# Performance work log

Measured on AMD Instinct MI355X. Metric: run time of the kernel, lower is better.

The kernel has to match this reference:

```python
import jax, jax.numpy as jnp
import numpy as np

N_NODES = 50000
N_EDGES = 400000
F_IN = 128
HID = 64
HEADS = 8
N_CLASSES = 16
NEG_SLOPE = 0.2  # PyG GATConv default negative_slope


def _glorot(key, shape):
    fan_in, fan_out = shape[0], shape[-1]
    lim = jnp.sqrt(6.0 / (fan_in + fan_out))
    return jax.random.uniform(key, shape, jnp.float32, -lim, lim)


def setup_inputs() -> dict:
    key = jax.random.key(0)
    ks = jax.random.split(key, 16)
    x = jax.random.normal(ks[0], (N_NODES, F_IN), jnp.float32)
    edge_index = jax.random.randint(ks[1], (2, N_EDGES), 0, N_NODES, jnp.int64)
    # layer 0: F_IN -> HEADS*HID (concat)
    W0 = _glorot(ks[2], (F_IN, HEADS * HID))
    a_s0 = _glorot(ks[3], (HEADS, HID))
    a_d0 = _glorot(ks[4], (HEADS, HID))
    b0 = jnp.zeros((HEADS * HID,), jnp.float32)
    # layer 1: HEADS*HID -> HEADS*HID (concat)
    W1 = _glorot(ks[5], (HEADS * HID, HEADS * HID))
    a_s1 = _glorot(ks[6], (HEADS, HID))
    a_d1 = _glorot(ks[7], (HEADS, HID))
    b1 = jnp.zeros((HEADS * HID,), jnp.float32)
    # final layer: HEADS*HID -> N_CLASSES, heads=1, concat=False (mean over heads)
    W2 = _glorot(ks[8], (HEADS * HID, 1 * N_CLASSES))
    a_s2 = _glorot(ks[9], (1, N_CLASSES))
    a_d2 = _glorot(ks[10], (1, N_CLASSES))
    b2 = jnp.zeros((N_CLASSES,), jnp.float32)
    return {"x": x, "edge_index": edge_index,
            "W0": W0, "a_s0": a_s0, "a_d0": a_d0, "b0": b0,
            "W1": W1, "a_s1": a_s1, "a_d1": a_d1, "b1": b1,
            "W2": W2, "a_s2": a_s2, "a_d2": a_d2, "b2": b2}


def gat_conv(x, src, dst, W, a_src, a_dst, b, num_nodes, concat):
    """One PyG-style GATConv (self-loops already in src/dst).
    x: [N, F_in]; W: [F_in, H*C]; a_src/a_dst: [H, C]; b: [H*C] or [C]."""
    H, C = a_src.shape
    h = (x @ W).reshape(num_nodes, H, C)                    # [N,H,C]
    al_s = jnp.einsum('nhc,hc->nh', h, a_src)               # [N,H]
    al_d = jnp.einsum('nhc,hc->nh', h, a_dst)               # [N,H]
    e = jax.nn.leaky_relu(al_s[src] + al_d[dst], NEG_SLOPE) # [E,H]
    # scatter-softmax over incoming edges of each destination node
    m = jax.ops.segment_max(e, dst, num_segments=num_nodes)  # [N,H]
    ex = jnp.exp(e - m[dst])
    denom = jax.ops.segment_sum(ex, dst, num_segments=num_nodes)
    alpha = ex / denom[dst]                                  # [E,H]
    out = jax.ops.segment_sum(alpha[:, :, None] * h[src], dst,
                              num_segments=num_nodes)        # [N,H,C]
    if concat:
        return out.reshape(num_nodes, H * C) + b
    return out.mean(axis=1) + b


def reference(x, edge_index, W0, a_s0, a_d0, b0, W1, a_s1, a_d1, b1,
              W2, a_s2, a_d2, b2):
    N = x.shape[0]
    # PyG GATConv adds self-loops by default
    loops = jnp.arange(N, dtype=edge_index.dtype)
    src = jnp.concatenate([edge_index[0], loops])
    dst = jnp.concatenate([edge_index[1], loops])
    h = gat_conv(x, src, dst, W0, a_s0, a_d0, b0, N, concat=True)
    h = jax.nn.elu(h)  # dropout is identity in eval mode
    h = gat_conv(h, src, dst, W1, a_s1, a_d1, b1, N, concat=True)
    h = jax.nn.elu(h)
    return gat_conv(h, src, dst, W2, a_s2, a_d2, b2, N, concat=False)
```

## Files before the change

### kernel.cpp

```cpp
#include <hip/hip_runtime.h>

#define N_NODES 50000
#define N_EDGES 400000
#define E_TOT   450000
#define NEG 0.2f
#define NB_SCAN ((N_NODES + 255) / 256)
#define MAXD 64

typedef unsigned short ushort_t;
typedef __attribute__((ext_vector_type(8))) _Float16 half8;
typedef __attribute__((ext_vector_type(4))) float  f32x4;
typedef __attribute__((ext_vector_type(8))) unsigned short ushort8;

__device__ __forceinline__ ushort_t f2h(float f){
    _Float16 h = (_Float16)f;
    union { _Float16 h; ushort_t u; } v; v.h = h; return v.u;
}
__device__ __forceinline__ float h_lo(unsigned u){
    union { unsigned u; _Float16 h[2]; } v; v.u = u; return (float)v.h[0];
}
__device__ __forceinline__ float h_hi(unsigned u){
    union { unsigned u; _Float16 h[2]; } v; v.u = u; return (float)v.h[1];
}
__device__ __forceinline__ void gload_lds16(const void* g, void* l){
    __builtin_amdgcn_global_load_lds((const __attribute__((address_space(1))) void*)g,
                                     (__attribute__((address_space(3))) void*)l, 16, 0, 0);
}
__device__ __forceinline__ int wave_incl_scan(int v, int lane){
    #pragma unroll
    for(int off = 1; off < 64; off <<= 1){
        int t = __shfl_up(v, off, 64);
        if(lane >= off) v += t;
    }
    return v;
}


__global__ void zero_ints(int* p, int n){
    int i = blockIdx.x*256 + threadIdx.x;
    if(i < n) p[i] = 0;
}

__global__ void count_deg(const int* __restrict__ ei, int* __restrict__ deg){
    int e = blockIdx.x*256 + threadIdx.x;
    if(e >= E_TOT) return;
    int dst = (e < N_EDGES) ? ei[N_EDGES + e] : (e - N_EDGES);
    atomicAdd(&deg[dst], 1);
}

__global__ void deg_block_sum(const int* __restrict__ deg, int* __restrict__ bsum){
    int i = blockIdx.x*256 + threadIdx.x;
    int lane = threadIdx.x & 63, wave = threadIdx.x >> 6;
    int v = (i < N_NODES) ? deg[i] : 0;
    #pragma unroll
    for(int off = 1; off < 64; off <<= 1) v += __shfl_xor(v, off, 64);
    __shared__ int sw[4];
    if(lane == 0) sw[wave] = v;
    __syncthreads();
    if(threadIdx.x == 0) bsum[blockIdx.x] = sw[0] + sw[1] + sw[2] + sw[3];
}

__global__ void scan_bsum(int* __restrict__ bsum, int* __restrict__ rowptr){
    int lane = threadIdx.x & 63, wave = threadIdx.x >> 6;
    int v = (threadIdx.x < NB_SCAN) ? bsum[threadIdx.x] : 0;
    int incl = wave_incl_scan(v, lane);
    __shared__ int sw[4];
    if(lane == 63) sw[wave] = incl;
    __syncthreads();
    int add = 0;
    for(int w = 0; w < wave; w++) add += sw[w];
    int excl = incl - v + add;
    if(threadIdx.x < NB_SCAN) bsum[threadIdx.x] = excl;
    if(threadIdx.x == 255) rowptr[N_NODES] = excl + v;
}

__global__ void scan_apply(const int* __restrict__ bsum,
                           int* __restrict__ dw, int* __restrict__ rowptr){
    int i = blockIdx.x*256 + threadIdx.x;
    int lane = threadIdx.x & 63, wave = threadIdx.x >> 6;
    int v = (i < N_NODES) ? dw[i] : 0;
    int incl = wave_incl_scan(v, lane);
    __shared__ int sw[4];
    if(lane == 63) sw[wave] = incl;
    __syncthreads();
    int add = bsum[blockIdx.x];
    for(int w = 0; w < wave; w++) add += sw[w];
    int excl = incl - v + add;
    if(i < N_NODES){ rowptr[i] = excl; dw[i] = excl; }
}

__global__ void scatter_edges(const int* __restrict__ ei, int* __restrict__ wofs,
                              int* __restrict__ csr){
    int e = blockIdx.x*256 + threadIdx.x;
    if(e >= E_TOT) return;
    int src, dst;
    if(e < N_EDGES){ src = ei[e]; dst = ei[N_EDGES + e]; }
    else { src = dst = e - N_EDGES; }
    int pos = atomicAdd(&wofs[dst], 1);
    csr[pos] = src;
}


__global__ void cvt_all(const float* __restrict__ x, const float* __restrict__ W0,
                        const float* __restrict__ W1,
                        ushort_t* __restrict__ xbf, ushort_t* __restrict__ W0t,
                        ushort_t* __restrict__ W1t){
    int i = blockIdx.x*256 + threadIdx.x;
    if(i < N_NODES*128) xbf[i] = f2h(x[i]);
    if(i < 512*128){ int n = i >> 7, k = i & 127; W0t[i] = f2h(W0[(size_t)k*512 + n]); }
    if(i < 512*512){ int n = i >> 9, k = i & 511; W1t[i] = f2h(W1[(size_t)k*512 + n]); }
}


template<int K>
__global__ __launch_bounds__(256) void gemm_bt(const ushort_t* __restrict__ A,
                                               const ushort_t* __restrict__ Bt,
                                               ushort_t* __restrict__ Cb,
                                               const float* __restrict__ a_s,
                                               const float* __restrict__ a_d,
                                               float* __restrict__ als,
                                               float* __restrict__ ald, int M){
    __shared__ ushort_t As[128*32];
    __shared__ ushort_t Bs[128*32];
    int tid  = threadIdx.x;
    int wave = tid >> 6, lane = tid & 63;
    int wm = wave & 1, wn = wave >> 1;
    int row0 = blockIdx.y * 128;
    int col0 = blockIdx.x * 128;

    f32x4 acc[4][4] = {};

    int lrow = lane >> 2;
    int lchk = (lane & 3) * 8;

    for(int kt = 0; kt < K; kt += 32){
        #pragma unroll
        for(int s = 0; s < 2; s++){
            int seg = wave*2 + s;
            int ar = row0 + seg*16 + lrow;
            ar = ar < M ? ar : M-1;
            gload_lds16(A  + (size_t)ar*K + kt + lchk, As + seg*512);
            int br = col0 + seg*16 + lrow;
            gload_lds16(Bt + (size_t)br*K + kt + lchk, Bs + seg*512);
        }
        __syncthreads();

        half8 a[4], b[4];
        int fm = lane & 15, fq = (lane >> 4) * 8;
        #pragma unroll
        for(int t = 0; t < 4; t++){
            a[t] = *(const half8*)&As[(wm*64 + t*16 + fm)*32 + fq];
            b[t] = *(const half8*)&Bs[(wn*64 + t*16 + fm)*32 + fq];
        }
        #pragma unroll
        for(int i = 0; i < 4; i++)
            #pragma unroll
            for(int j = 0; j < 4; j++)
                acc[i][j] = __builtin_amdgcn_mfma_f32_16x16x32_f16(a[i], b[j], acc[i][j], 0, 0, 0);
        __syncthreads();
    }

    int cm = (lane >> 4) * 4, cn = lane & 15;
    int head = (col0 + wn*64) >> 6;
    float as_[4], ad_[4];
    #pragma unroll
    for(int j = 0; j < 4; j++){
        int c = head*64 + cn + j*16;
        as_[j] = a_s[c]; ad_[j] = a_d[c];
    }
    #pragma unroll
    for(int i = 0; i < 4; i++){
        #pragma unroll
        for(int p = 0; p < 4; p++){
            int r = row0 + wm*64 + i*16 + cm + p;
            float ps = 0.f, pd = 0.f;
            if(r < M){
                ushort_t* cp = &Cb[(size_t)r*512 + col0 + wn*64 + cn];
                #pragma unroll
                for(int j = 0; j < 4; j++){
                    float v = acc[i][j][p];
                    cp[j*16] = f2h(v);
                    ps += v*as_[j]; pd += v*ad_[j];
                }
            }
            #pragma unroll
            for(int off = 1; off < 16; off <<= 1){
                ps += __shfl_xor(ps, off);
                pd += __shfl_xor(pd, off);
            }
            if(cn == 0 && r < M){ als[r*8 + head] = ps; ald[r*8 + head] = pd; }
        }
    }
}


__global__ __launch_bounds__(256) void attn_agg(const ushort_t* __restrict__ h,
        const float* __restrict__ als, const float* __restrict__ ald,
        const int* __restrict__ rowptr, const int* __restrict__ csr,
        const float* __restrict__ bias, ushort_t* __restrict__ out){
    __shared__ float sm[4][8], sd[4][8];
    __shared__ float sex[4][MAXD][8];
    int wv = threadIdx.x >> 6, lane = threadIdx.x & 63;
    int n = blockIdx.x*4 + wv;
    int start = rowptr[n], end = rowptr[n+1];

    int hd = lane & 7, e8 = lane >> 3;
    float aldv = ald[n*8 + hd];
    float lmax = -1e30f;
    for(int idx = start + e8; idx < end; idx += 8){
        int e = idx - start;
        int src = csr[idx];
        float v = als[src*8 + hd] + aldv;
        v = v > 0.f ? v : NEG*v;
        if(e < MAXD) sex[wv][e][hd] = v;
        lmax = fmaxf(lmax, v);
    }
    for(int off = 8; off < 64; off <<= 1) lmax = fmaxf(lmax, __shfl_xor(lmax, off));
    float lsum = 0.f;
    for(int idx = start + e8; idx < end; idx += 8){
        int e = idx - start;
        float v;
        if(e < MAXD) v = sex[wv][e][hd];
        else { int src = csr[idx]; v = als[src*8 + hd] + aldv; v = v > 0.f ? v : NEG*v; }
        float ex = __expf(v - lmax);
        if(e < MAXD) sex[wv][e][hd] = ex;
        lsum += ex;
    }
    for(int off = 8; off < 64; off <<= 1) lsum += __shfl_xor(lsum, off);
    if(lane < 8){ sm[wv][hd] = lmax; sd[wv][hd] = 1.f / lsum; }
    __syncthreads();

    int head = lane >> 3;
    float inv = sd[wv][head];
    float acc[8] = {};

    int cnt = end - start;
    int nmain = cnt < MAXD ? cnt : MAXD;
    int mend = start + nmain;
    int last = mend - 1;
    for(int idx = start; idx < mend; idx += 4){
        int j1 = idx+1, j2 = idx+2, j3 = idx+3;
        int s0 = csr[idx];
        int s1 = csr[j1 <= last ? j1 : last];
        int s2 = csr[j2 <= last ? j2 : last];
        int s3 = csr[j3 <= last ? j3 : last];
        uint4 p0 = *(const uint4*)&h[(size_t)s0*512 + lane*8];
        uint4 p1 = *(const uint4*)&h[(size_t)s1*512 + lane*8];
        uint4 p2 = *(const uint4*)&h[(size_t)s2*512 + lane*8];
        uint4 p3 = *(const uint4*)&h[(size_t)s3*512 + lane*8];
        float e0 = sex[wv][idx -start][head];
        float e1 = (j1 < mend) ? sex[wv][j1-start][head] : 0.f;
        float e2 = (j2 < mend) ? sex[wv][j2-start][head] : 0.f;
        float e3 = (j3 < mend) ? sex[wv][j3-start][head] : 0.f;
        acc[0] += e0*h_lo(p0.x) + e1*h_lo(p1.x) + e2*h_lo(p2.x) + e3*h_lo(p3.x);
        acc[1] += e0*h_hi(p0.x) + e1*h_hi(p1.x) + e2*h_hi(p2.x) + e3*h_hi(p3.x);
        acc[2] += e0*h_lo(p0.y) + e1*h_lo(p1.y) + e2*h_lo(p2.y) + e3*h_lo(p3.y);
        acc[3] += e0*h_hi(p0.y) + e1*h_hi(p1.y) + e2*h_hi(p2.y) + e3*h_hi(p3.y);
        acc[4] += e0*h_lo(p0.z) + e1*h_lo(p1.z) + e2*h_lo(p2.z) + e3*h_lo(p3.z);
        acc[5] += e0*h_hi(p0.z) + e1*h_hi(p1.z) + e2*h_hi(p2.z) + e3*h_hi(p3.z);
        acc[6] += e0*h_lo(p0.w) + e1*h_lo(p1.w) + e2*h_lo(p2.w) + e3*h_lo(p3.w);
        acc[7] += e0*h_hi(p0.w) + e1*h_hi(p1.w) + e2*h_hi(p2.w) + e3*h_hi(p3.w);
    }
    if(mend < end){
        float m = sm[wv][head];
        float aldn = ald[n*8 + head];
        for(int idx = mend; idx < end; idx++){
            int src = csr[idx];
            float v = als[src*8 + head] + aldn;
            v = v > 0.f ? v : NEG*v;
            float e0 = __expf(v - m);
            uint4 p = *(const uint4*)&h[(size_t)src*512 + lane*8];
            acc[0] += e0*h_lo(p.x); acc[1] += e0*h_hi(p.x);
            acc[2] += e0*h_lo(p.y); acc[3] += e0*h_hi(p.y);
            acc[4] += e0*h_lo(p.z); acc[5] += e0*h_hi(p.z);
            acc[6] += e0*h_lo(p.w); acc[7] += e0*h_hi(p.w);
        }
    }

    ushort8 o;
    #pragma unroll
    for(int j = 0; j < 8; j++){
        float v = acc[j]*inv + bias[lane*8 + j];
        v = v > 0.f ? v : (__expf(v) - 1.f);
        o[j] = f2h(v);
    }
    *(ushort8*)&out[(size_t)n*512 + lane*8] = o;
}


__global__ __launch_bounds__(256) void gemm2_k(const ushort_t* __restrict__ A,
                                               const float* __restrict__ W,
                                               const float* __restrict__ a_s2,
                                               const float* __restrict__ a_d2,
                                               float* __restrict__ C,
                                               float* __restrict__ als,
                                               float* __restrict__ ald){
    __shared__ float Ws[16][513];
    for(int i = threadIdx.x; i < 512*16; i += 256){
        int k = i >> 4, c = i & 15;
        Ws[c][k] = W[i];
    }
    __syncthreads();
    int t = blockIdx.x*256 + threadIdx.x;
    int c = t & 15;
    long row = t >> 4;
    const ushort_t* ap = &A[row*512];
    const float* wp = &Ws[c][0];
    float acc = 0.f;
    for(int k = 0; k < 512; k += 8){
        uint4 p = *(const uint4*)&ap[k];
        acc += h_lo(p.x)*wp[k+0] + h_hi(p.x)*wp[k+1]
             + h_lo(p.y)*wp[k+2] + h_hi(p.y)*wp[k+3]
             + h_lo(p.z)*wp[k+4] + h_hi(p.z)*wp[k+5]
             + h_lo(p.w)*wp[k+6] + h_hi(p.w)*wp[k+7];
    }
    C[t] = acc;
    float ps = acc * a_s2[c], pd = acc * a_d2[c];
    #pragma unroll
    for(int off = 1; off < 16; off <<= 1){
        ps += __shfl_xor(ps, off);
        pd += __shfl_xor(pd, off);
    }
    if(c == 0){ als[row] = ps; ald[row] = pd; }
}

__global__ __launch_bounds__(256) void attn_agg2(const float* __restrict__ h2,
        const float* __restrict__ als, const float* __restrict__ ald,
        const int* __restrict__ rowptr, const int* __restrict__ csr,
        const float* __restrict__ b2, float* __restrict__ out){
    int wv = threadIdx.x >> 6, lane = threadIdx.x & 63;
    int q = lane >> 4, c = lane & 15;
    int n = blockIdx.x*16 + wv*4 + q;
    int start = rowptr[n], end = rowptr[n+1];
    float aldv = ald[n];

    float lmax = -1e30f;
    for(int idx = start + c; idx < end; idx += 16){
        float v = als[csr[idx]] + aldv; v = v > 0.f ? v : NEG*v;
        lmax = fmaxf(lmax, v);
    }
    #pragma unroll
    for(int off = 1; off < 16; off <<= 1) lmax = fmaxf(lmax, __shfl_xor(lmax, off));
    float lsum = 0.f;
    for(int idx = start + c; idx < end; idx += 16){
        float v = als[csr[idx]] + aldv; v = v > 0.f ? v : NEG*v;
        lsum += __expf(v - lmax);
    }
    #pragma unroll
    for(int off = 1; off < 16; off <<= 1) lsum += __shfl_xor(lsum, off);
    float inv = 1.f / lsum;

    float acc = 0.f;
    for(int idx = start; idx < end; idx++){
        int src = csr[idx];
        float v = als[src] + aldv; v = v > 0.f ? v : NEG*v;
        float alpha = __expf(v - lmax) * inv;
        acc += alpha * h2[src*16 + c];
    }
    out[n*16 + c] = acc + b2[c];
}


extern "C" void kernel_launch(void* const* d_in, const int* in_sizes, int n_in,
                              void* d_out, int out_size, void* d_ws, size_t ws_size,
                              hipStream_t stream) {
    const float* x    = (const float*)d_in[0];
    const int*   ei   = (const int*)  d_in[1];
    const float* W0   = (const float*)d_in[2];
    const float* a_s0 = (const float*)d_in[3];
    const float* a_d0 = (const float*)d_in[4];
    const float* b0   = (const float*)d_in[5];
    const float* W1   = (const float*)d_in[6];
    const float* a_s1 = (const float*)d_in[7];
    const float* a_d1 = (const float*)d_in[8];
    const float* b1   = (const float*)d_in[9];
    const float* W2   = (const float*)d_in[10];
    const float* a_s2 = (const float*)d_in[11];
    const float* a_d2 = (const float*)d_in[12];
    const float* b2   = (const float*)d_in[13];
    float* out = (float*)d_out;

    char* w = (char*)d_ws;
    auto alloc = [&](size_t bytes){ void* p = (void*)w; w += (bytes + 255) & ~(size_t)255; return p; };
    int*      rowptr = (int*)     alloc((N_NODES+1)*sizeof(int));
    int*      wofs   = (int*)     alloc(N_NODES*sizeof(int));
    int*      bsum   = (int*)     alloc(NB_SCAN*sizeof(int));
    int*      csr    = (int*)     alloc(E_TOT*sizeof(int));
    float*    als    = (float*)   alloc((size_t)N_NODES*8*sizeof(float));
    float*    ald    = (float*)   alloc((size_t)N_NODES*8*sizeof(float));
    ushort_t* hb     = (ushort_t*)alloc((size_t)N_NODES*512*sizeof(ushort_t));
    ushort_t* hbf    = (ushort_t*)alloc((size_t)N_NODES*512*sizeof(ushort_t));
    ushort_t* xbf    = (ushort_t*)alloc((size_t)N_NODES*128*sizeof(ushort_t));
    ushort_t* W0t    = (ushort_t*)alloc((size_t)512*128*sizeof(ushort_t));
    ushort_t* W1t    = (ushort_t*)alloc((size_t)512*512*sizeof(ushort_t));
    float*    h2     = (float*)   alloc((size_t)N_NODES*16*sizeof(float));

    zero_ints<<<(N_NODES+255)/256, 256, 0, stream>>>(wofs, N_NODES);
    count_deg<<<(E_TOT+255)/256, 256, 0, stream>>>(ei, wofs);
    deg_block_sum<<<NB_SCAN, 256, 0, stream>>>(wofs, bsum);
    scan_bsum<<<1, 256, 0, stream>>>(bsum, rowptr);
    scan_apply<<<NB_SCAN, 256, 0, stream>>>(bsum, wofs, rowptr);
    scatter_edges<<<(E_TOT+255)/256, 256, 0, stream>>>(ei, wofs, csr);

    cvt_all<<<(N_NODES*128+255)/256, 256, 0, stream>>>(x, W0, W1, xbf, W0t, W1t);

    gemm_bt<128><<<dim3(4, (N_NODES+127)/128), 256, 0, stream>>>(xbf, W0t, hb, a_s0, a_d0, als, ald, N_NODES);
    attn_agg<<<N_NODES/4, 256, 0, stream>>>(hb, als, ald, rowptr, csr, b0, hbf);

    gemm_bt<512><<<dim3(4, (N_NODES+127)/128), 256, 0, stream>>>(hbf, W1t, hb, a_s1, a_d1, als, ald, N_NODES);
    attn_agg<<<N_NODES/4, 256, 0, stream>>>(hb, als, ald, rowptr, csr, b1, hbf);

    gemm2_k<<<(N_NODES*16)/256, 256, 0, stream>>>(hbf, W2, a_s2, a_d2, h2, als, ald);
    attn_agg2<<<N_NODES/16, 256, 0, stream>>>(h2, als, ald, rowptr, csr, b2, out);
}
```

Before: 463.9 us.

## Stage GEMM output through LDS for coalesced stores and trim setup launches

The GEMM epilogue now writes its fp16 tile into a padded shared buffer that reuses the A/B staging space. It then stores each row with 16-byte vector writes instead of scattered 2-byte stores, aiming to make output writes coalesced. Separately, zeroing the degree array is folded into the conversion kernel, and the single-block scan of block sums is removed: each scan_apply block instead sums its preceding block totals directly. This cuts two kernel launches at the cost of some redundant reads and extra barriers in the GEMM epilogue.

```diff
diff --git a/kernel.cpp b/kernel.cpp
--- a/kernel.cpp
+++ b/kernel.cpp
@@ -36,11 +36,6 @@
 }
 
 
-__global__ void zero_ints(int* p, int n){
-    int i = blockIdx.x*256 + threadIdx.x;
-    if(i < n) p[i] = 0;
-}
-
 __global__ void count_deg(const int* __restrict__ ei, int* __restrict__ deg){
     int e = blockIdx.x*256 + threadIdx.x;
     if(e >= E_TOT) return;
@@ -60,33 +55,28 @@
     if(threadIdx.x == 0) bsum[blockIdx.x] = sw[0] + sw[1] + sw[2] + sw[3];
 }
 
-__global__ void scan_bsum(int* __restrict__ bsum, int* __restrict__ rowptr){
+__global__ void scan_apply(const int* __restrict__ bsum,
+                           int* __restrict__ dw, int* __restrict__ rowptr){
+    __shared__ int soff;
+    __shared__ int sw[4];
+    int i = blockIdx.x*256 + threadIdx.x;
     int lane = threadIdx.x & 63, wave = threadIdx.x >> 6;
-    int v = (threadIdx.x < NB_SCAN) ? bsum[threadIdx.x] : 0;
+    if(wave == 0){
+        int s = 0;
+        for(int j = lane; j < (int)blockIdx.x; j += 64) s += bsum[j];
+        #pragma unroll
+        for(int off = 1; off < 64; off <<= 1) s += __shfl_xor(s, off, 64);
+        if(lane == 0) soff = s;
+    }
+    int v = (i < N_NODES) ? dw[i] : 0;
     int incl = wave_incl_scan(v, lane);
-    __shared__ int sw[4];
     if(lane == 63) sw[wave] = incl;
     __syncthreads();
-    int add = 0;
-    for(int w = 0; w < wave; w++) add += sw[w];
-    int excl = incl - v + add;
-    if(threadIdx.x < NB_SCAN) bsum[threadIdx.x] = excl;
-    if(threadIdx.x == 255) rowptr[N_NODES] = excl + v;
-}
-
-__global__ void scan_apply(const int* __restrict__ bsum,
-                           int* __restrict__ dw, int* __restrict__ rowptr){
-    int i = blockIdx.x*256 + threadIdx.x;
-    int lane = threadIdx.x & 63, wave = threadIdx.x >> 6;
-    int v = (i < N_NODES) ? dw[i] : 0;
-    int incl = wave_incl_scan(v, lane);
-    __shared__ int sw[4];
-    if(lane == 63) sw[wave] = incl;
-    __syncthreads();
-    int add = bsum[blockIdx.x];
+    int add = soff;
     for(int w = 0; w < wave; w++) add += sw[w];
     int excl = incl - v + add;
     if(i < N_NODES){ rowptr[i] = excl; dw[i] = excl; }
+    if(i == N_NODES-1) rowptr[N_NODES] = excl + v;
 }
 
 __global__ void scatter_edges(const int* __restrict__ ei, int* __restrict__ wofs,
@@ -104,11 +94,12 @@
 __global__ void cvt_all(const float* __restrict__ x, const float* __restrict__ W0,
                         const float* __restrict__ W1,
                         ushort_t* __restrict__ xbf, ushort_t* __restrict__ W0t,
-                        ushort_t* __restrict__ W1t){
+                        ushort_t* __restrict__ W1t, int* __restrict__ wofs){
     int i = blockIdx.x*256 + threadIdx.x;
     if(i < N_NODES*128) xbf[i] = f2h(x[i]);
     if(i < 512*128){ int n = i >> 7, k = i & 127; W0t[i] = f2h(W0[(size_t)k*512 + n]); }
     if(i < 512*512){ int n = i >> 9, k = i & 511; W1t[i] = f2h(W1[(size_t)k*512 + n]); }
+    if(i < N_NODES) wofs[i] = 0;
 }
 
 
@@ -120,8 +111,9 @@
                                                const float* __restrict__ a_d,
                                                float* __restrict__ als,
                                                float* __restrict__ ald, int M){
-    __shared__ ushort_t As[128*32];
-    __shared__ ushort_t Bs[128*32];
+    __shared__ ushort_t buf[128*72];
+    ushort_t* As = buf;
+    ushort_t* Bs = buf + 4096;
     int tid  = threadIdx.x;
     int wave = tid >> 6, lane = tid & 63;
     int wm = wave & 1, wn = wave >> 1;
@@ -175,11 +167,9 @@
             int r = row0 + wm*64 + i*16 + cm + p;
             float ps = 0.f, pd = 0.f;
             if(r < M){
-                ushort_t* cp = &Cb[(size_t)r*512 + col0 + wn*64 + cn];
                 #pragma unroll
                 for(int j = 0; j < 4; j++){
                     float v = acc[i][j][p];
-                    cp[j*16] = f2h(v);
                     ps += v*as_[j]; pd += v*ad_[j];
                 }
             }
@@ -190,6 +180,32 @@
             }
             if(cn == 0 && r < M){ als[r*8 + head] = ps; ald[r*8 + head] = pd; }
         }
+    }
+
+    #pragma unroll
+    for(int pass = 0; pass < 2; pass++){
+        if(wn == pass){
+            #pragma unroll
+            for(int i = 0; i < 4; i++)
+                #pragma unroll
+                for(int p = 0; p < 4; p++){
+                    int lr = wm*64 + i*16 + cm + p;
+                    #pragma unroll
+                    for(int j = 0; j < 4; j++)
+                        buf[lr*72 + j*16 + cn] = f2h(acc[i][j][p]);
+                }
+        }
+        __syncthreads();
+        int row = tid >> 1;
+        int hc  = (tid & 1) * 32;
+        int r = row0 + row;
+        if(r < M){
+            ushort_t* gp = &Cb[(size_t)r*512 + col0 + pass*64 + hc];
+            #pragma unroll
+            for(int k = 0; k < 4; k++)
+                *(ushort8*)&gp[k*8] = *(const ushort8*)&buf[row*72 + hc + k*8];
+        }
+        __syncthreads();
     }
 }
 
@@ -395,15 +411,13 @@
     ushort_t* W1t    = (ushort_t*)alloc((size_t)512*512*sizeof(ushort_t));
     float*    h2     = (float*)   alloc((size_t)N_NODES*16*sizeof(float));
 
-    zero_ints<<<(N_NODES+255)/256, 256, 0, stream>>>(wofs, N_NODES);
+    cvt_all<<<(N_NODES*128+255)/256, 256, 0, stream>>>(x, W0, W1, xbf, W0t, W1t, wofs);
+
     count_deg<<<(E_TOT+255)/256, 256, 0, stream>>>(ei, wofs);
     deg_block_sum<<<NB_SCAN, 256, 0, stream>>>(wofs, bsum);
-    scan_bsum<<<1, 256, 0, stream>>>(bsum, rowptr);
     scan_apply<<<NB_SCAN, 256, 0, stream>>>(bsum, wofs, rowptr);
     scatter_edges<<<(E_TOT+255)/256, 256, 0, stream>>>(ei, wofs, csr);
 
-    cvt_all<<<(N_NODES*128+255)/256, 256, 0, stream>>>(x, W0, W1, xbf, W0t, W1t);
-
     gemm_bt<128><<<dim3(4, (N_NODES+127)/128), 256, 0, stream>>>(xbf, W0t, hb, a_s0, a_d0, als, ald, N_NODES);
     attn_agg<<<N_NODES/4, 256, 0, stream>>>(hb, als, ald, rowptr, csr, b0, hbf);
 
```

After: 484.3 us. 4.4% more time.
